# Kernel optimization log

Measured on AMD Instinct MI355X. Metric: run time of the kernel, lower is better.

## Reference

```python
import jax, jax.numpy as jnp
import numpy as np

C = 1024
CI = 256  # in_channels // inter_ratio
BN_EPS = 1e-5


def setup_inputs() -> dict:
    key = jax.random.key(0)
    ks = jax.random.split(key, 12)
    B, H, W = 16, 64, 32
    xavier = lambda k, o, i: jax.random.uniform(k, (o, i), jnp.float32,
                                                -np.sqrt(6.0 / (o + i)), np.sqrt(6.0 / (o + i)))
    return {
        "x": jax.random.normal(ks[0], (B, C, H, W), jnp.float32),
        "theta_w": xavier(ks[1], CI, C), "theta_b": jnp.zeros((CI,), jnp.float32),
        "phi_w": xavier(ks[2], CI, C), "phi_b": jnp.zeros((CI,), jnp.float32),
        "g_w": xavier(ks[3], CI, C), "g_b": jnp.zeros((CI,), jnp.float32),
        "w_w": xavier(ks[4], C, CI), "w_b": jnp.zeros((C,), jnp.float32),
        # BatchNorm (inference-mode) params; random (not zero-init) so the block is non-trivial
        "bn_gamma": jax.random.normal(ks[5], (C,), jnp.float32) * 0.1 + 1.0,
        "bn_beta": jax.random.normal(ks[6], (C,), jnp.float32) * 0.1,
        "bn_mean": jax.random.normal(ks[7], (C,), jnp.float32) * 0.1,
        "bn_var": jax.random.uniform(ks[8], (C,), jnp.float32, 0.5, 1.5),
    }


def reference(x, theta_w, theta_b, phi_w, phi_b, g_w, g_b, w_w, w_b,
              bn_gamma, bn_beta, bn_mean, bn_var):
    B, Cc, H, W = x.shape
    N = H * W
    xf = x.reshape(B, Cc, N)  # [B, C, N]
    # 1x1 convs == channel GEMMs
    theta = jnp.einsum('oc,bcn->bno', theta_w, xf) + theta_b  # [B, N, Ci]
    phi = jnp.einsum('oc,bcn->bon', phi_w, xf) + phi_b[:, None]  # [B, Ci, N]
    g = jnp.einsum('oc,bcn->bno', g_w, xf) + g_b  # [B, N, Ci]
    attn = jax.nn.softmax(jnp.einsum('bno,bom->bnm', theta, phi), axis=-1)  # [B, N, N]
    y = jnp.einsum('bnm,bmo->bno', attn, g)  # [B, N, Ci]
    z = jnp.einsum('co,bno->bcn', w_w, y) + w_b[None, :, None]  # [B, C, N]
    inv = bn_gamma / jnp.sqrt(bn_var + BN_EPS)
    z = (z - bn_mean[None, :, None]) * inv[None, :, None] + bn_beta[None, :, None]
    return z.reshape(B, Cc, H, W) + x
```

## Files before the change

### kernel.cpp

```cpp
#include <hip/hip_runtime.h>
#include <cstdint>

#define BATCH 16
#define CH 1024
#define CIN 256
#define NSP 2048
#define BN_EPS 1e-5f

typedef _Float16 f16;
typedef f16   f16x4 __attribute__((ext_vector_type(4)));
typedef f16   f16x8 __attribute__((ext_vector_type(8)));
typedef float f32x4 __attribute__((ext_vector_type(4)));
typedef float f32x16 __attribute__((ext_vector_type(16)));

typedef __attribute__((address_space(3))) void lds_t;
typedef __attribute__((address_space(1))) const void gbl_t;

__device__ __forceinline__ void gld16(void* l, const void* g) {
    __builtin_amdgcn_global_load_lds((gbl_t*)g, (lds_t*)l, 16, 0, 0);
}

__global__ __launch_bounds__(256) void k_prep(
    const float* __restrict__ tw, const float* __restrict__ pw,
    const float* __restrict__ gw, const float* __restrict__ ww,
    const float* __restrict__ wb, const float* __restrict__ gamma,
    const float* __restrict__ beta, const float* __restrict__ mean,
    const float* __restrict__ var,
    f16* __restrict__ w_all, float* __restrict__ inv_out, float* __restrict__ off_out)
{
    int id = blockIdx.x * 256 + threadIdx.x;
    if (id < 4 * 262144) {
        int sel = id >> 18, off = id & 262143;
        const float* src = sel == 0 ? tw : sel == 1 ? pw : sel == 2 ? gw : ww;
        w_all[id] = (f16)src[off];
    } else {
        int c = id - 4 * 262144;
        if (c < CH) {
            float iv = gamma[c] * rsqrtf(var[c] + BN_EPS);
            inv_out[c] = iv;
            off_out[c] = (wb[c] - mean[c]) * iv + beta[c];
        }
    }
}

__global__ __launch_bounds__(256) void k_transpose_x(
    const float* __restrict__ x, f16* __restrict__ xT)
{
    __shared__ float tile[64 * 65];
    int t = threadIdx.x;
    int n0 = blockIdx.x * 64, c0 = blockIdx.y * 64, b = blockIdx.z;
    const float* xb = x + (size_t)b * CH * NSP;
    for (int k = 0; k < 4; ++k) {
        int id = t + 256 * k;
        int row = id >> 4, cc = id & 15;
        float4 v = *(const float4*)(xb + (size_t)(c0 + row) * NSP + n0 + cc * 4);
        tile[row * 65 + cc * 4 + 0] = v.x;
        tile[row * 65 + cc * 4 + 1] = v.y;
        tile[row * 65 + cc * 4 + 2] = v.z;
        tile[row * 65 + cc * 4 + 3] = v.w;
    }
    __syncthreads();
    f16* xTb = xT + (size_t)b * NSP * CH;
    for (int k = 0; k < 2; ++k) {
        int id = t + 256 * k;
        int n = id >> 3, c8 = id & 7;
        f16x8 o;
        #pragma unroll
        for (int j = 0; j < 8; ++j) o[j] = (f16)tile[(c8 * 8 + j) * 65 + n];
        *(f16x8*)(xTb + (size_t)(n0 + n) * CH + c0 + c8 * 8) = o;
    }
}

__global__ __launch_bounds__(256, 3) void k_qkv(
    const f16* __restrict__ xT, const f16* __restrict__ w_all,
    const float* __restrict__ tb, const float* __restrict__ pb,
    const float* __restrict__ gb,
    f16* __restrict__ theta, f16* __restrict__ phiT, f16* __restrict__ gT)
{
    __shared__ char smem[40960];
    f16* a_lds = (f16*)smem;
    f16* b_lds = (f16*)(smem + 8192);
    int t = threadIdx.x;
    int w = t >> 6, lane = t & 63, l15 = lane & 15, q = lane >> 4;
    int sw = l15 & 7;
    int n0 = blockIdx.x * 64, b = blockIdx.y, set = blockIdx.z;
    const f16* W  = w_all + (size_t)set * (CIN * CH);
    const f16* xA = xT + ((size_t)b * NSP + n0) * CH;

    int rA  = lane >> 3;
    int ccs = (lane & 7) ^ rA;

    f32x4 acc[4][4];
    #pragma unroll
    for (int i = 0; i < 4; ++i)
        #pragma unroll
        for (int j = 0; j < 4; ++j) acc[i][j] = (f32x4){0.f, 0.f, 0.f, 0.f};

    for (int it = 0; it < 16; ++it) {
        #pragma unroll
        for (int i = 0; i < 2; ++i) {
            int win = w * 2 + i;
            int n = win * 8 + rA;
            gld16((char*)a_lds + win * 1024,
                  xA + (size_t)n * CH + it * 64 + ccs * 8);
        }
        #pragma unroll
        for (int i = 0; i < 8; ++i) {
            int win = w * 8 + i;
            int o = win * 8 + rA;
            gld16((char*)b_lds + win * 1024,
                  W + (size_t)o * CH + it * 64 + ccs * 8);
        }
        __syncthreads();

        #pragma unroll
        for (int kl = 0; kl < 2; ++kl) {
            int c16 = kl * 4 + q;
            int pos = (c16 ^ sw) & 7;
            f16x8 af[4], bfr[4];
            #pragma unroll
            for (int tn = 0; tn < 4; ++tn)
                af[tn] = *(const f16x8*)(a_lds + (16 * tn + l15) * 64 + pos * 8);
            #pragma unroll
            for (int to = 0; to < 4; ++to)
                bfr[to] = *(const f16x8*)(b_lds + (64 * w + 16 * to + l15) * 64 + pos * 8);
            #pragma unroll
            for (int tn = 0; tn < 4; ++tn)
                #pragma unroll
                for (int to = 0; to < 4; ++to)
                    acc[tn][to] = __builtin_amdgcn_mfma_f32_16x16x32_f16(
                        af[tn], bfr[to], acc[tn][to], 0, 0, 0);
        }
        __syncthreads();
    }

    const float* bias = set == 0 ? tb : set == 1 ? pb : gb;
    float bv[4];
    #pragma unroll
    for (int to = 0; to < 4; ++to) bv[to] = bias[64 * w + 16 * to + l15];

    if (set < 2) {
        f16* e_lds = (f16*)smem;
        #pragma unroll
        for (int tn = 0; tn < 4; ++tn)
            #pragma unroll
            for (int to = 0; to < 4; ++to)
                #pragma unroll
                for (int r = 0; r < 4; ++r)
                    e_lds[(16 * tn + 4 * q + r) * 256 + 64 * w + 16 * to + l15] =
                        (f16)(acc[tn][to][r] + bv[to]);
        __syncthreads();
        f16* dst = (set == 0 ? theta : phiT) + ((size_t)b * NSP + n0) * CIN;
        for (int k2 = 0; k2 < 8; ++k2) {
            int id = t + 256 * k2;
            *(f16x8*)(dst + id * 8) = *(const f16x8*)(e_lds + id * 8);
        }
    } else {
        f16* e_lds = (f16*)smem;
        #pragma unroll
        for (int tn = 0; tn < 4; ++tn)
            #pragma unroll
            for (int to = 0; to < 4; ++to)
                #pragma unroll
                for (int r = 0; r < 4; ++r)
                    e_lds[(64 * w + 16 * to + l15) * 72 + 16 * tn + 4 * q + r] =
                        (f16)(acc[tn][to][r] + bv[to]);
        __syncthreads();
        f16* dst = gT + (size_t)b * CIN * NSP + n0;
        for (int k2 = 0; k2 < 8; ++k2) {
            int id = t + 256 * k2;
            int o = id >> 3, cc = id & 7;
            *(f16x8*)(dst + (size_t)o * NSP + cc * 8) = *(const f16x8*)(e_lds + o * 72 + cc * 8);
        }
    }
}

__global__ __launch_bounds__(256, 2) void k_attn(
    const f16* __restrict__ theta, const f16* __restrict__ phiT,
    const f16* __restrict__ gT, f16* __restrict__ y)
{
    __shared__ char smem[76544];
    f16* phi_lds = (f16*)smem;
    f16* g_lds   = (f16*)(smem + 32768);
    f16* p_lds   = (f16*)(smem + 65536);
    float* pmax_lds  = (float*)(smem + 75264);
    float* psum_lds  = (float*)(smem + 75776);
    float* alpha_lds = (float*)(smem + 76288);

    int t = threadIdx.x;
    int w = t >> 6, lane = t & 63;
    int l31 = lane & 31, hi = lane >> 5;
    int qh = w & 1, kh = w >> 1;
    int b = blockIdx.x, n0 = blockIdx.y * 64;

    const f16* thb  = theta + (size_t)b * NSP * CIN;
    const f16* phib = phiT + (size_t)b * NSP * CIN;
    const f16* gTb  = gT + (size_t)b * CIN * NSP;

    f16x8 th[16];
    {
        const f16* tp = thb + (size_t)(n0 + qh * 32 + l31) * CIN + 8 * hi;
        #pragma unroll
        for (int s = 0; s < 16; ++s) th[s] = *(const f16x8*)(tp + s * 16);
    }

    f32x16 acc[2][2];
    #pragma unroll
    for (int i = 0; i < 2; ++i)
        #pragma unroll
        for (int j = 0; j < 2; ++j)
            #pragma unroll
            for (int r = 0; r < 16; ++r) acc[i][j][r] = 0.f;
    float m_run = -INFINITY, l_run = 0.f;

    int p_cdst = lane & 31;
    int g_rin = lane >> 3, g_cdst = lane & 7;

    #define DMA_PHI(IT)                                                         \
        _Pragma("unroll")                                                       \
        for (int i_ = 0; i_ < 8; ++i_) {                                        \
            int win_ = w * 8 + i_;                                              \
            int row_ = win_ * 2 + hi;                                           \
            int cs_ = (p_cdst & 24) | ((p_cdst ^ row_) & 7);                    \
            gld16((char*)phi_lds + win_ * 1024,                                 \
                  phib + (size_t)((IT) * 64 + row_) * CIN + cs_ * 8);           \
        }
    #define DMA_G(IT)                                                           \
        _Pragma("unroll")                                                       \
        for (int i_ = 0; i_ < 8; ++i_) {                                        \
            int win_ = w * 8 + i_;                                              \
            int row_ = win_ * 8 + g_rin;                                        \
            int cs_ = g_cdst ^ (row_ & 7);                                      \
            gld16((char*)g_lds + win_ * 1024,                                   \
                  gTb + (size_t)row_ * NSP + (IT) * 64 + cs_ * 8);              \
        }

    DMA_PHI(0)
    DMA_G(0)
    __syncthreads();

    int srow = kh * 32 + l31;
    int qrow = qh * 32 + l31;
    int mli  = kh * 64 + qrow;

    for (int it = 0; it < 32; ++it) {
        f32x16 sacc;
        #pragma unroll
        for (int r = 0; r < 16; ++r) sacc[r] = 0.f;
        #pragma unroll
        for (int s = 0; s < 16; ++s) {
            int ch = 2 * s + hi;
            int slot = (ch & 24) | ((ch ^ srow) & 7);
            f16x8 af = *(const f16x8*)(phi_lds + srow * 256 + slot * 8);
            sacc = __builtin_amdgcn_mfma_f32_32x32x16_f16(af, th[s], sacc, 0, 0, 0);
        }

        float tmax = sacc[0];
        #pragma unroll
        for (int r = 1; r < 16; ++r) tmax = fmaxf(tmax, sacc[r]);
        tmax = fmaxf(tmax, __shfl_xor(tmax, 32));
        if (lane < 32) pmax_lds[mli] = tmax;
        __syncthreads();

        float tile_max = fmaxf(tmax, pmax_lds[mli ^ 64]);
        float mnew  = fmaxf(m_run, tile_max);
        float alpha = __expf(m_run - mnew);
        m_run = mnew;
        float rs = 0.f;
        float pv[16];
        #pragma unroll
        for (int r = 0; r < 16; ++r) {
            pv[r] = __expf(sacc[r] - mnew);
            rs += pv[r];
        }
        rs += __shfl_xor(rs, 32);
        if (lane < 32) {
            psum_lds[mli] = rs;
            if (kh == 0) alpha_lds[qrow] = alpha;
        }
        #pragma unroll
        for (int g4 = 0; g4 < 4; ++g4) {
            f16x4 pk = { (f16)pv[4*g4+0], (f16)pv[4*g4+1], (f16)pv[4*g4+2], (f16)pv[4*g4+3] };
            *(f16x4*)(p_lds + qrow * 76 + kh * 32 + 8 * g4 + 4 * hi) = pk;
        }
        __syncthreads();

        if (it < 31) DMA_PHI(it + 1)

        l_run = l_run * alpha + rs + psum_lds[mli ^ 64];

        f32x4 av[2][4];
        float mn = 1.0f;
        #pragma unroll
        for (int Mt = 0; Mt < 2; ++Mt)
            #pragma unroll
            for (int g4 = 0; g4 < 4; ++g4) {
                av[Mt][g4] = *(const f32x4*)(alpha_lds + Mt * 32 + 8 * g4 + 4 * hi);
                mn = fminf(mn, fminf(fminf(av[Mt][g4][0], av[Mt][g4][1]),
                                     fminf(av[Mt][g4][2], av[Mt][g4][3])));
            }
        if (__any(mn < 1.0f)) {
            #pragma unroll
            for (int Mt = 0; Mt < 2; ++Mt)
                #pragma unroll
                for (int g4 = 0; g4 < 4; ++g4)
                    #pragma unroll
                    for (int rr = 0; rr < 4; ++rr) {
                        acc[Mt][0][4*g4+rr] *= av[Mt][g4][rr];
                        acc[Mt][1][4*g4+rr] *= av[Mt][g4][rr];
                    }
        }

        #pragma unroll
        for (int ks = 0; ks < 4; ++ks) {
            f16x8 pa0 = *(const f16x8*)(p_lds + l31 * 76 + ks * 16 + 8 * hi);
            f16x8 pa1 = *(const f16x8*)(p_lds + (32 + l31) * 76 + ks * 16 + 8 * hi);
            int slot = (2 * ks + hi) ^ (l31 & 7);
            f16x8 gb0 = *(const f16x8*)(g_lds + (64 * w + l31) * 64 + slot * 8);
            f16x8 gb1 = *(const f16x8*)(g_lds + (64 * w + 32 + l31) * 64 + slot * 8);
            acc[0][0] = __builtin_amdgcn_mfma_f32_32x32x16_f16(pa0, gb0, acc[0][0], 0, 0, 0);
            acc[0][1] = __builtin_amdgcn_mfma_f32_32x32x16_f16(pa0, gb1, acc[0][1], 0, 0, 0);
            acc[1][0] = __builtin_amdgcn_mfma_f32_32x32x16_f16(pa1, gb0, acc[1][0], 0, 0, 0);
            acc[1][1] = __builtin_amdgcn_mfma_f32_32x32x16_f16(pa1, gb1, acc[1][1], 0, 0, 0);
        }
        __syncthreads();

        if (it < 31) DMA_G(it + 1)
    }

    if (lane < 32 && kh == 0) alpha_lds[qrow] = 1.0f / l_run;
    __syncthreads();
    f16* e_lds = (f16*)smem;
    #pragma unroll
    for (int Mt = 0; Mt < 2; ++Mt)
        #pragma unroll
        for (int g4 = 0; g4 < 4; ++g4) {
            f32x4 lv = *(const f32x4*)(alpha_lds + Mt * 32 + 8 * g4 + 4 * hi);
            #pragma unroll
            for (int rr = 0; rr < 4; ++rr) {
                int q = Mt * 32 + 8 * g4 + 4 * hi + rr;
                #pragma unroll
                for (int Nt = 0; Nt < 2; ++Nt) {
                    int cin = 64 * w + Nt * 32 + l31;
                    e_lds[q * 264 + cin] = (f16)(acc[Mt][Nt][4*g4+rr] * lv[rr]);
                }
            }
        }
    __syncthreads();
    f16* dst = y + ((size_t)b * NSP + n0) * CIN;
    for (int k2 = 0; k2 < 8; ++k2) {
        int id = t + 256 * k2;
        int row = id >> 5, cc = id & 31;
        *(f16x8*)(dst + (size_t)row * CIN + cc * 8) = *(const f16x8*)(e_lds + row * 264 + cc * 8);
    }
    #undef DMA_PHI
    #undef DMA_G
}

__global__ __launch_bounds__(256, 3) void k_out(
    const f16* __restrict__ yv, const f16* __restrict__ ww,
    const float* __restrict__ inv, const float* __restrict__ off,
    const float* __restrict__ x, float* __restrict__ out)
{
    __shared__ char smem[40960];
    f16*   a_lds = (f16*)smem;
    f16*   b_lds = (f16*)(smem + 8192);
    float* z_lds = (float*)smem;
    int t = threadIdx.x;
    int w = t >> 6, lane = t & 63, l15 = lane & 15, q = lane >> 4;
    int sw = l15 & 7;
    int n0 = blockIdx.x * 64, cb = blockIdx.y * 256, b = blockIdx.z;

    const f16* yA = yv + ((size_t)b * NSP + n0) * CIN;
    const f16* W  = ww + (size_t)cb * CIN;

    int rA  = lane >> 3;
    int ccs = (lane & 7) ^ rA;

    f32x4 acc[4][4];
    #pragma unroll
    for (int i = 0; i < 4; ++i)
        #pragma unroll
        for (int j = 0; j < 4; ++j) acc[i][j] = (f32x4){0.f, 0.f, 0.f, 0.f};

    for (int it = 0; it < 4; ++it) {
        #pragma unroll
        for (int i = 0; i < 2; ++i) {
            int win = w * 2 + i;
            int n = win * 8 + rA;
            gld16((char*)a_lds + win * 1024,
                  yA + (size_t)n * CIN + it * 64 + ccs * 8);
        }
        #pragma unroll
        for (int i = 0; i < 8; ++i) {
            int win = w * 8 + i;
            int o = win * 8 + rA;
            gld16((char*)b_lds + win * 1024,
                  W + (size_t)o * CIN + it * 64 + ccs * 8);
        }
        __syncthreads();

        #pragma unroll
        for (int kl = 0; kl < 2; ++kl) {
            int c16 = kl * 4 + q;
            int pos = (c16 ^ sw) & 7;
            f16x8 af[4], bfr[4];
            #pragma unroll
            for (int tn = 0; tn < 4; ++tn)
                af[tn] = *(const f16x8*)(a_lds + (16 * tn + l15) * 64 + pos * 8);
            #pragma unroll
            for (int to = 0; to < 4; ++to)
                bfr[to] = *(const f16x8*)(b_lds + (64 * w + 16 * to + l15) * 64 + pos * 8);
            #pragma unroll
            for (int tn = 0; tn < 4; ++tn)
                #pragma unroll
                for (int to = 0; to < 4; ++to)
                    acc[tn][to] = __builtin_amdgcn_mfma_f32_16x16x32_f16(
                        af[tn], bfr[to], acc[tn][to], 0, 0, 0);
        }
        __syncthreads();
    }

    float4 xv[4];
    #pragma unroll
    for (int k2 = 0; k2 < 4; ++k2) {
        int f = t + 256 * k2;
        int zrr = f >> 4, nn4 = f & 15;
        int c = cb + 64 * (zrr >> 4) + (zrr & 15);
        xv[k2] = *(const float4*)(x + ((size_t)b * CH + c) * NSP + n0 + nn4 * 4);
    }

    #pragma unroll
    for (int to = 0; to < 4; ++to) {
        #pragma unroll
        for (int tn = 0; tn < 4; ++tn)
            #pragma unroll
            for (int r = 0; r < 4; ++r)
                z_lds[(16 * w + l15) * 68 + 16 * tn + 4 * q + r] = acc[tn][to][r];
        __syncthreads();

        float4 nxt[4];
        if (to < 3) {
            #pragma unroll
            for (int k2 = 0; k2 < 4; ++k2) {
                int f = t + 256 * k2;
                int zrr = f >> 4, nn4 = f & 15;
                int c = cb + 64 * (zrr >> 4) + 16 * (to + 1) + (zrr & 15);
                nxt[k2] = *(const float4*)(x + ((size_t)b * CH + c) * NSP + n0 + nn4 * 4);
            }
        }

        #pragma unroll
        for (int k2 = 0; k2 < 4; ++k2) {
            int f = t + 256 * k2;
            int zrr = f >> 4, nn4 = f & 15;
            int c = cb + 64 * (zrr >> 4) + 16 * to + (zrr & 15);
            float4 z = *(const float4*)(z_lds + zrr * 68 + nn4 * 4);
            float iv = inv[c], ov = off[c];
            size_t idx = ((size_t)b * CH + c) * NSP + n0 + nn4 * 4;
            float4 o;
            o.x = z.x * iv + ov + xv[k2].x;
            o.y = z.y * iv + ov + xv[k2].y;
            o.z = z.z * iv + ov + xv[k2].z;
            o.w = z.w * iv + ov + xv[k2].w;
            *(float4*)(out + idx) = o;
        }

        if (to < 3) {
            #pragma unroll
            for (int k2 = 0; k2 < 4; ++k2) xv[k2] = nxt[k2];
            __syncthreads();
        }
    }
}

extern "C" void kernel_launch(void* const* d_in, const int* in_sizes, int n_in,
                              void* d_out, int out_size, void* d_ws, size_t ws_size,
                              hipStream_t stream)
{
    const float* x     = (const float*)d_in[0];
    const float* tw    = (const float*)d_in[1];
    const float* tb    = (const float*)d_in[2];
    const float* pw    = (const float*)d_in[3];
    const float* pb    = (const float*)d_in[4];
    const float* gw    = (const float*)d_in[5];
    const float* gb_   = (const float*)d_in[6];
    const float* ww    = (const float*)d_in[7];
    const float* wb    = (const float*)d_in[8];
    const float* gamma = (const float*)d_in[9];
    const float* beta  = (const float*)d_in[10];
    const float* mean  = (const float*)d_in[11];
    const float* var   = (const float*)d_in[12];
    float* out = (float*)d_out;

    char* ws = (char*)d_ws;
    f16* xT    = (f16*)ws;
    f16* theta = (f16*)(ws + 67108864);
    f16* phiT  = (f16*)(ws + 83886080);
    f16* gT    = (f16*)(ws + 100663296);
    f16* yv    = (f16*)(ws + 117440512);
    f16* w_all = (f16*)(ws + 134217728);
    float* inv  = (float*)(ws + 136314880);
    float* offv = (float*)(ws + 136318976);

    k_prep<<<4100, 256, 0, stream>>>(tw, pw, gw, ww, wb, gamma, beta, mean, var,
                                     w_all, inv, offv);
    k_transpose_x<<<dim3(32, 16, 16), 256, 0, stream>>>(x, xT);
    k_qkv<<<dim3(32, 16, 3), 256, 0, stream>>>(xT, w_all, tb, pb, gb_, theta, phiT, gT);
    k_attn<<<dim3(16, 32), 256, 0, stream>>>(theta, phiT, gT, yv);
    k_out<<<dim3(32, 4, 16), 256, 0, stream>>>(yv, w_all + 3 * 262144, inv, offv, x, out);
}
```

Before: 480.4 us.

## Prefetch g tile into registers early and restructure attention loop synchronization

The attention kernel now issues the next g tile's global loads into registers at the start of each iteration and writes them to LDS after the PV MMAs, replacing the direct global-to-LDS DMA issued at the end. The phi prefetch moves earlier, right after the first barrier. __syncthreads becomes explicit waitcnt plus s_barrier, and MFMA phases are wrapped in s_setprio. The QK^T chain is split into two independent accumulators to shorten the dependency chain, and the P tile pitch drops from 76 to 72, shrinking LDS. The aim is to hide global latency behind compute, at the cost of extra VGPRs and an added barrier per iteration, which could hurt occupancy.

```diff
diff --git a/kernel.cpp b/kernel.cpp
--- a/kernel.cpp
+++ b/kernel.cpp
@@ -179,13 +179,13 @@
     const f16* __restrict__ theta, const f16* __restrict__ phiT,
     const f16* __restrict__ gT, f16* __restrict__ y)
 {
-    __shared__ char smem[76544];
+    __shared__ char smem[76032];
     f16* phi_lds = (f16*)smem;
     f16* g_lds   = (f16*)(smem + 32768);
     f16* p_lds   = (f16*)(smem + 65536);
-    float* pmax_lds  = (float*)(smem + 75264);
-    float* psum_lds  = (float*)(smem + 75776);
-    float* alpha_lds = (float*)(smem + 76288);
+    float* pmax_lds  = (float*)(smem + 74752);
+    float* psum_lds  = (float*)(smem + 75264);
+    float* alpha_lds = (float*)(smem + 75776);
 
     int t = threadIdx.x;
     int w = t >> 6, lane = t & 63;
@@ -215,6 +215,7 @@
 
     int p_cdst = lane & 31;
     int g_rin = lane >> 3, g_cdst = lane & 7;
+    int gc8 = t & 7, grb = t >> 3;
 
     #define DMA_PHI(IT)                                                         \
         _Pragma("unroll")                                                       \
@@ -225,42 +226,63 @@
             gld16((char*)phi_lds + win_ * 1024,                                 \
                   phib + (size_t)((IT) * 64 + row_) * CIN + cs_ * 8);           \
         }
-    #define DMA_G(IT)                                                           \
+    #define DMA_G0()                                                            \
         _Pragma("unroll")                                                       \
         for (int i_ = 0; i_ < 8; ++i_) {                                        \
             int win_ = w * 8 + i_;                                              \
             int row_ = win_ * 8 + g_rin;                                        \
             int cs_ = g_cdst ^ (row_ & 7);                                      \
             gld16((char*)g_lds + win_ * 1024,                                   \
-                  gTb + (size_t)row_ * NSP + (IT) * 64 + cs_ * 8);              \
+                  gTb + (size_t)row_ * NSP + cs_ * 8);                          \
         }
 
     DMA_PHI(0)
-    DMA_G(0)
-    __syncthreads();
+    DMA_G0()
+    asm volatile("s_waitcnt vmcnt(0)" ::: "memory");
+    __builtin_amdgcn_s_barrier();
 
     int srow = kh * 32 + l31;
     int qrow = qh * 32 + l31;
     int mli  = kh * 64 + qrow;
 
+    f16x8 gr[8];
+
     for (int it = 0; it < 32; ++it) {
-        f32x16 sacc;
-        #pragma unroll
-        for (int r = 0; r < 16; ++r) sacc[r] = 0.f;
-        #pragma unroll
-        for (int s = 0; s < 16; ++s) {
-            int ch = 2 * s + hi;
-            int slot = (ch & 24) | ((ch ^ srow) & 7);
-            f16x8 af = *(const f16x8*)(phi_lds + srow * 256 + slot * 8);
-            sacc = __builtin_amdgcn_mfma_f32_32x32x16_f16(af, th[s], sacc, 0, 0, 0);
-        }
+        if (it < 31) {
+            #pragma unroll
+            for (int j = 0; j < 8; ++j)
+                gr[j] = *(const f16x8*)(gTb + (size_t)(grb + 32 * j) * NSP
+                                        + (it + 1) * 64 + gc8 * 8);
+        }
+        __builtin_amdgcn_sched_barrier(0);
+
+        f32x16 s0, s1;
+        #pragma unroll
+        for (int r = 0; r < 16; ++r) { s0[r] = 0.f; s1[r] = 0.f; }
+        __builtin_amdgcn_s_setprio(1);
+        #pragma unroll
+        for (int s = 0; s < 8; ++s) {
+            int ch0 = 2 * s + hi;
+            int sl0 = (ch0 & 24) | ((ch0 ^ srow) & 7);
+            f16x8 a0 = *(const f16x8*)(phi_lds + srow * 256 + sl0 * 8);
+            s0 = __builtin_amdgcn_mfma_f32_32x32x16_f16(a0, th[s], s0, 0, 0, 0);
+            int ch1 = 2 * (s + 8) + hi;
+            int sl1 = (ch1 & 24) | ((ch1 ^ srow) & 7);
+            f16x8 a1 = *(const f16x8*)(phi_lds + srow * 256 + sl1 * 8);
+            s1 = __builtin_amdgcn_mfma_f32_32x32x16_f16(a1, th[s + 8], s1, 0, 0, 0);
+        }
+        __builtin_amdgcn_s_setprio(0);
+        f32x16 sacc = s0 + s1;
 
         float tmax = sacc[0];
         #pragma unroll
         for (int r = 1; r < 16; ++r) tmax = fmaxf(tmax, sacc[r]);
         tmax = fmaxf(tmax, __shfl_xor(tmax, 32));
         if (lane < 32) pmax_lds[mli] = tmax;
-        __syncthreads();
+        asm volatile("s_waitcnt lgkmcnt(0)" ::: "memory");
+        __builtin_amdgcn_s_barrier();
+
+        if (it < 31) DMA_PHI(it + 1)
 
         float tile_max = fmaxf(tmax, pmax_lds[mli ^ 64]);
         float mnew  = fmaxf(m_run, tile_max);
@@ -281,11 +303,10 @@
         #pragma unroll
         for (int g4 = 0; g4 < 4; ++g4) {
             f16x4 pk = { (f16)pv[4*g4+0], (f16)pv[4*g4+1], (f16)pv[4*g4+2], (f16)pv[4*g4+3] };
-            *(f16x4*)(p_lds + qrow * 76 + kh * 32 + 8 * g4 + 4 * hi) = pk;
-        }
-        __syncthreads();
-
-        if (it < 31) DMA_PHI(it + 1)
+            *(f16x4*)(p_lds + qrow * 72 + kh * 32 + 8 * g4 + 4 * hi) = pk;
+        }
+        asm volatile("s_waitcnt lgkmcnt(0)" ::: "memory");
+        __builtin_amdgcn_s_barrier();
 
         l_run = l_run * alpha + rs + psum_lds[mli ^ 64];
 
@@ -311,10 +332,11 @@
                     }
         }
 
+        __builtin_amdgcn_s_setprio(1);
         #pragma unroll
         for (int ks = 0; ks < 4; ++ks) {
-            f16x8 pa0 = *(const f16x8*)(p_lds + l31 * 76 + ks * 16 + 8 * hi);
-            f16x8 pa1 = *(const f16x8*)(p_lds + (32 + l31) * 76 + ks * 16 + 8 * hi);
+            f16x8 pa0 = *(const f16x8*)(p_lds + l31 * 72 + ks * 16 + 8 * hi);
+            f16x8 pa1 = *(const f16x8*)(p_lds + (32 + l31) * 72 + ks * 16 + 8 * hi);
             int slot = (2 * ks + hi) ^ (l31 & 7);
             f16x8 gb0 = *(const f16x8*)(g_lds + (64 * w + l31) * 64 + slot * 8);
             f16x8 gb1 = *(const f16x8*)(g_lds + (64 * w + 32 + l31) * 64 + slot * 8);
@@ -323,9 +345,20 @@
             acc[1][0] = __builtin_amdgcn_mfma_f32_32x32x16_f16(pa1, gb0, acc[1][0], 0, 0, 0);
             acc[1][1] = __builtin_amdgcn_mfma_f32_32x32x16_f16(pa1, gb1, acc[1][1], 0, 0, 0);
         }
-        __syncthreads();
-
-        if (it < 31) DMA_G(it + 1)
+        __builtin_amdgcn_s_setprio(0);
+        asm volatile("s_waitcnt lgkmcnt(0)" ::: "memory");
+        __builtin_amdgcn_s_barrier();
+
+        if (it < 31) {
+            asm volatile("s_waitcnt vmcnt(8)" ::: "memory");
+            #pragma unroll
+            for (int j = 0; j < 8; ++j) {
+                int o = grb + 32 * j;
+                *(f16x8*)(g_lds + o * 64 + (gc8 ^ (o & 7)) * 8) = gr[j];
+            }
+            asm volatile("s_waitcnt vmcnt(0) lgkmcnt(0)" ::: "memory");
+            __builtin_amdgcn_s_barrier();
+        }
     }
 
     if (lane < 32 && kh == 0) alpha_lds[qrow] = 1.0f / l_run;
@@ -354,7 +387,7 @@
         *(f16x8*)(dst + (size_t)row * CIN + cc * 8) = *(const f16x8*)(e_lds + row * 264 + cc * 8);
     }
     #undef DMA_PHI
-    #undef DMA_G
+    #undef DMA_G0
 }
 
 __global__ __launch_bounds__(256, 3) void k_out(
```

New measurement: 471.2 us. No clear change (-1.9%).
